# Kernel tuning notes

Measured on AMD Instinct MI355X. Metric: run time of the kernel, lower is better.

Reference implementation:

```python
import jax, jax.numpy as jnp
import numpy as np

B, T, C, H = 4, 2048, 1024, 16
D = C // H


def setup_inputs() -> dict:
    key = jax.random.key(0)
    ks = jax.random.split(key, 6)
    s = 1.0 / np.sqrt(C)
    return {
        "x": jax.random.normal(ks[0], (B, T, C), dtype=jnp.float32),
        "attention_mask": jnp.ones((B, 1, T), dtype=jnp.int32),
        "Wq": jax.random.normal(ks[1], (C, C), dtype=jnp.float32) * s,
        "bq": jnp.zeros((C,), dtype=jnp.float32),
        "Wk": jax.random.normal(ks[2], (C, C), dtype=jnp.float32) * s,
        "bk": jnp.zeros((C,), dtype=jnp.float32),
        "Wv": jax.random.normal(ks[3], (C, C), dtype=jnp.float32) * s,
        "bv": jnp.zeros((C,), dtype=jnp.float32),
        "Wp": jax.random.normal(ks[4], (C, C), dtype=jnp.float32) * s,
        "bp": jnp.zeros((C,), dtype=jnp.float32),
    }


def reference(x, attention_mask, Wq, bq, Wk, bk, Wv, bv, Wp, bp):
    b, t, c = x.shape
    d = c // H
    # projections (torch Linear: x @ W^T + b)
    q = (x @ Wq.T + bq).reshape(b, t, H, d).transpose(0, 2, 1, 3)  # [B,H,T,D]
    k = (x @ Wk.T + bk).reshape(b, t, H, d).transpose(0, 2, 1, 3)
    v = (x @ Wv.T + bv).reshape(b, t, H, d).transpose(0, 2, 1, 3)
    attn = jnp.einsum("bhqd,bhkd->bhqk", q, k) / jnp.sqrt(jnp.asarray(d, x.dtype))
    mask = attention_mask[:, :, :t]  # [B,1,T] -> broadcast over [B,H,T,T] keys
    attn = jnp.where(mask[:, :, None, :] == 0, jnp.asarray(-jnp.inf, x.dtype), attn)
    attn = jax.nn.softmax(attn, axis=-1)  # dropout p=0 (eval)
    y = jnp.einsum("bhqk,bhkd->bhqd", attn, v)
    y = y.transpose(0, 2, 1, 3).reshape(b, t, c)
    return y @ Wp.T + bp
```

## Files before the change

### kernel.cpp

```cpp
#include <hip/hip_runtime.h>


#define TT 2048
#define CC 1024
#define HH 16
#define DD 64
#define BB 4

typedef unsigned short u16;
typedef unsigned int u32;
typedef __attribute__((ext_vector_type(8))) short bf16x8;
typedef __attribute__((ext_vector_type(4))) float f32x4;

#if __has_builtin(__builtin_amdgcn_exp2f)
#define EXP2(x) __builtin_amdgcn_exp2f(x)
#else
#define EXP2(x) __expf((x) * 0.6931471805599453f)
#endif

__device__ __forceinline__ u16 f2bf(float f) {
    u32 u = __builtin_bit_cast(u32, f);
    u += 0x7FFFu + ((u >> 16) & 1u);
    return (u16)(u >> 16);
}
__device__ __forceinline__ u32 pk2(float a, float b) {
    u32 ua = __builtin_bit_cast(u32, a); ua += 0x7FFFu + ((ua >> 16) & 1u);
    u32 ub = __builtin_bit_cast(u32, b); ub += 0x7FFFu + ((ub >> 16) & 1u);
    return __builtin_amdgcn_perm(ub, ua, 0x07060302);
}

#define GLDS(g, l) __builtin_amdgcn_global_load_lds( \
    (const __attribute__((address_space(1))) void*)(g), \
    (__attribute__((address_space(3))) void*)(l), 16, 0, 0)

__global__ __launch_bounds__(256) void wcvt(const float* __restrict__ s,
                                            u16* __restrict__ d, int n8) {
    const int i = blockIdx.x * 256 + threadIdx.x;
    if (i < n8) {
        const float4 f0 = ((const float4*)s)[2 * i];
        const float4 f1 = ((const float4*)s)[2 * i + 1];
        uint4 w;
        w.x = pk2(f0.x, f0.y); w.y = pk2(f0.z, f0.w);
        w.z = pk2(f1.x, f1.y); w.w = pk2(f1.z, f1.w);
        ((uint4*)d)[i] = w;
    }
}

__global__ __launch_bounds__(256) void wcvt3(const float* __restrict__ s0,
                                             const float* __restrict__ s1,
                                             const float* __restrict__ s2,
                                             u16* __restrict__ d0,
                                             u16* __restrict__ d1,
                                             u16* __restrict__ d2, int n8) {
    const int which = blockIdx.y;
    const float* s = (which == 0) ? s0 : (which == 1) ? s1 : s2;
    u16* d = (which == 0) ? d0 : (which == 1) ? d1 : d2;
    const int i = blockIdx.x * 256 + threadIdx.x;
    if (i < n8) {
        const float4 f0 = ((const float4*)s)[2 * i];
        const float4 f1 = ((const float4*)s)[2 * i + 1];
        uint4 w;
        w.x = pk2(f0.x, f0.y); w.y = pk2(f0.z, f0.w);
        w.z = pk2(f1.x, f1.y); w.w = pk2(f1.z, f1.w);
        ((uint4*)d)[i] = w;
    }
}

template <int PROJ>
__global__ __launch_bounds__(256) void gemmX(const u16* __restrict__ A,
                                             const u16* __restrict__ Wb,
                                             const float* __restrict__ b0,
                                             const float* __restrict__ b1,
                                             const float* __restrict__ b2,
                                             void* __restrict__ out0,
                                             void* __restrict__ out1,
                                             void* __restrict__ out2) {
    __shared__ u16 As[128 * 64];
    __shared__ u16 Bs[128 * 64];

    const int tid  = threadIdx.x;
    const int wave = tid >> 6, lane = tid & 63;
    const int quad = lane >> 4, l16 = lane & 15;
    const int bm = blockIdx.y * 128, bn = blockIdx.x * 128;
    const int wm = (wave >> 1) * 64, wn = (wave & 1) * 64;
    const int K = CC;

    f32x4 acc[4][4] = {};

    for (int k0 = 0; k0 < K; k0 += 64) {
#pragma unroll
        for (int rr = 0; rr < 4; rr++) {
            const int c = rr * 256 + tid;
            const int row = c >> 3;
            const int cs = ((c & 7) ^ (row & 7)) * 8;
            GLDS(&Wb[(size_t)(bn + row) * K + k0 + cs], &Bs[c * 8]);
        }
#pragma unroll
        for (int rr = 0; rr < 4; rr++) {
            const int c = rr * 256 + tid;
            const int row = c >> 3;
            const int cs = ((c & 7) ^ (row & 7)) * 8;
            GLDS(&A[(size_t)(bm + row) * K + k0 + cs], &As[c * 8]);
        }
        __syncthreads();

#pragma unroll
        for (int ks = 0; ks < 2; ks++) {
            bf16x8 af[4], bfr[4];
#pragma unroll
            for (int i = 0; i < 4; i++) {
                const int row = wm + i * 16 + l16;
                const int s8 = (ks * 4 + quad) ^ (row & 7);
                af[i] = *(bf16x8*)&As[row * 64 + s8 * 8];
            }
#pragma unroll
            for (int j = 0; j < 4; j++) {
                const int row = wn + j * 16 + l16;
                const int s8 = (ks * 4 + quad) ^ (row & 7);
                bfr[j] = *(bf16x8*)&Bs[row * 64 + s8 * 8];
            }
#pragma unroll
            for (int i = 0; i < 4; i++)
#pragma unroll
                for (int j = 0; j < 4; j++)
                    acc[i][j] = __builtin_amdgcn_mfma_f32_16x16x32_bf16(af[i], bfr[j], acc[i][j], 0, 0, 0);
        }
        __syncthreads();
    }

    if (PROJ) {
        float* out = (float*)out0;
#pragma unroll
        for (int j = 0; j < 4; j++) {
            const int col = bn + wn + j * 16 + l16;
            const float bv = b0[col];
#pragma unroll
            for (int i = 0; i < 4; i++) {
                const int row0 = bm + wm + i * 16 + quad * 4;
#pragma unroll
                for (int r = 0; r < 4; r++)
                    out[(size_t)(row0 + r) * CC + col] = acc[i][j][r] + bv;
            }
        }
    } else {
        const int mid = bn >> 10;
        const float* bias = (mid == 0) ? b0 : (mid == 1) ? b1 : b2;
#pragma unroll
        for (int j = 0; j < 4; j++) {
            const int col  = bn + wn + j * 16 + l16;
            const int colL = col & (CC - 1);
            const float bv = bias[colL];
#pragma unroll
            for (int i = 0; i < 4; i++) {
                const int row0 = bm + wm + i * 16 + quad * 4;
                if (mid < 2) {
                    u16* out = (u16*)(mid ? out1 : out0);
#pragma unroll
                    for (int r = 0; r < 4; r++)
                        out[(size_t)(row0 + r) * CC + colL] = f2bf(acc[i][j][r] + bv);
                } else {
                    const int hh = colL >> 6, dch = colL & 63;
                    const int bb = row0 >> 11, t0 = row0 & (TT - 1);
                    const size_t idx = (((size_t)bb * HH + hh) * DD + dch) * TT + t0;
                    uint2 w;
                    w.x = pk2(acc[i][j][0] + bv, acc[i][j][1] + bv);
                    w.y = pk2(acc[i][j][2] + bv, acc[i][j][3] + bv);
                    *(uint2*)&((u16*)out2)[idx] = w;
                }
            }
        }
    }
}

__global__ __launch_bounds__(256) void attn(const u16* __restrict__ Q,
                                            const u16* __restrict__ Kb,
                                            const u16* __restrict__ Vt,
                                            const int* __restrict__ mask,
                                            u16* __restrict__ Y) {
    const int b = blockIdx.z, h = blockIdx.y, qt = blockIdx.x;
    const int tid  = threadIdx.x;
    const int wave = tid >> 6, lane = tid & 63;
    const int quad = lane >> 4, l16 = lane & 15;
    const int qrow0 = qt * 128 + wave * 32;

    __shared__ u16 Ks[64 * 64];
    __shared__ u16 Vs[64 * 64];
    __shared__ u16 Plds[4][32][72];

    const size_t qb = ((size_t)b * TT + qrow0) * CC + h * DD;

    bf16x8 qf[2][2];
#pragma unroll
    for (int m = 0; m < 2; m++)
#pragma unroll
        for (int ks = 0; ks < 2; ks++)
            qf[m][ks] = *(const bf16x8*)&Q[qb + (size_t)(m * 16 + l16) * CC + ks * 32 + quad * 8];

    const int c0 = tid, c1 = tid + 256;
    const int r0 = c0 >> 3, r1 = c1 >> 3;
    const int kp0 = (c0 & 7) ^ ((r0 >> 2) & 7), kp1 = (c1 & 7) ^ ((r1 >> 2) & 7);
    const int vp0 = (c0 & 7) ^ (r0 & 7),        vp1 = (c1 & 7) ^ (r1 & 7);
    const u16* kgp = Kb + ((size_t)b * TT) * CC + h * DD;
    const u16* vgp = Vt + ((size_t)(b * HH + h) * DD) * TT;
    const int* mp = mask + b * TT + 4 * l16;

    f32x4 o[2][4] = {};
    float lsum[2][4] = {};
    const float SC = 0.18033688011112042f;

#pragma unroll 1
    for (int kt = 0; kt < TT; kt += 64) {
        GLDS(&kgp[(size_t)(kt + r0) * CC + kp0 * 8], &Ks[c0 * 8]);
        GLDS(&kgp[(size_t)(kt + r1) * CC + kp1 * 8], &Ks[c1 * 8]);
        GLDS(&vgp[(size_t)r0 * TT + kt + vp0 * 8], &Vs[c0 * 8]);
        GLDS(&vgp[(size_t)r1 * TT + kt + vp1 * 8], &Vs[c1 * 8]);
        __syncthreads();

        f32x4 s[2][4] = {};
#pragma unroll
        for (int n = 0; n < 4; n++) {
#pragma unroll
            for (int ks = 0; ks < 2; ks++) {
                const int krow = 4 * l16 + n;
                const int pos = (ks * 4 + quad) ^ ((krow >> 2) & 7);
                const bf16x8 kf = *(bf16x8*)&Ks[krow * 64 + pos * 8];
#pragma unroll
                for (int m = 0; m < 2; m++)
                    s[m][n] = __builtin_amdgcn_mfma_f32_16x16x32_bf16(qf[m][ks], kf, s[m][n], 0, 0, 0);
            }
        }

        const int4 mv = *(const int4*)&mp[kt];
        float bb[4];
        bb[0] = mv.x ? 0.f : -1e38f;
        bb[1] = mv.y ? 0.f : -1e38f;
        bb[2] = mv.z ? 0.f : -1e38f;
        bb[3] = mv.w ? 0.f : -1e38f;

#pragma unroll
        for (int m = 0; m < 2; m++)
#pragma unroll
            for (int r = 0; r < 4; r++) {
                const float p0 = EXP2(fmaf(s[m][0][r], SC, bb[0]));
                const float p1 = EXP2(fmaf(s[m][1][r], SC, bb[1]));
                const float p2 = EXP2(fmaf(s[m][2][r], SC, bb[2]));
                const float p3 = EXP2(fmaf(s[m][3][r], SC, bb[3]));
                lsum[m][r] += (p0 + p1) + (p2 + p3);
                uint2 w; w.x = pk2(p0, p1); w.y = pk2(p2, p3);
                *(uint2*)&Plds[wave][m * 16 + quad * 4 + r][4 * l16] = w;
            }

#pragma unroll
        for (int ks = 0; ks < 2; ks++) {
            bf16x8 pf[2];
#pragma unroll
            for (int m = 0; m < 2; m++)
                pf[m] = *(bf16x8*)&Plds[wave][m * 16 + l16][ks * 32 + quad * 8];
#pragma unroll
            for (int dt = 0; dt < 4; dt++) {
                const int vrow = dt * 16 + l16;
                const int pos = (ks * 4 + quad) ^ (vrow & 7);
                const bf16x8 vf = *(bf16x8*)&Vs[vrow * 64 + pos * 8];
#pragma unroll
                for (int m = 0; m < 2; m++)
                    o[m][dt] = __builtin_amdgcn_mfma_f32_16x16x32_bf16(pf[m], vf, o[m][dt], 0, 0, 0);
            }
        }
        __syncthreads();
    }

#pragma unroll
    for (int off = 1; off < 16; off <<= 1)
#pragma unroll
        for (int m = 0; m < 2; m++)
#pragma unroll
            for (int r = 0; r < 4; r++) lsum[m][r] += __shfl_xor(lsum[m][r], off, 64);

#pragma unroll
    for (int m = 0; m < 2; m++) {
        float inv[4];
#pragma unroll
        for (int r = 0; r < 4; r++) inv[r] = 1.0f / lsum[m][r];
#pragma unroll
        for (int dt = 0; dt < 4; dt++)
#pragma unroll
            for (int r = 0; r < 4; r++)
                Y[qb + (size_t)(m * 16 + quad * 4 + r) * CC + dt * 16 + l16] = f2bf(o[m][dt][r] * inv[r]);
    }
}

extern "C" void kernel_launch(void* const* d_in, const int* in_sizes, int n_in,
                              void* d_out, int out_size, void* d_ws, size_t ws_size,
                              hipStream_t stream) {
    const float* x    = (const float*)d_in[0];
    const int*   mask = (const int*)d_in[1];
    const float* Wq   = (const float*)d_in[2];
    const float* bq   = (const float*)d_in[3];
    const float* Wk   = (const float*)d_in[4];
    const float* bk   = (const float*)d_in[5];
    const float* Wv   = (const float*)d_in[6];
    const float* bv   = (const float*)d_in[7];
    const float* Wp   = (const float*)d_in[8];
    const float* bp   = (const float*)d_in[9];

    u16* ws = (u16*)d_ws;
    const size_t sz = (size_t)BB * TT * CC;
    u16* Qb   = ws;
    u16* Kbuf = ws + sz;
    u16* Vtb  = ws + 2 * sz;

    u16* xb   = (u16*)d_out;
    u16* Wq16 = xb + sz;
    u16* Wk16 = Wq16 + (size_t)CC * CC;
    u16* Wv16 = Wk16 + (size_t)CC * CC;

    const int W8 = CC * CC / 8;
    wcvt<<<4096, 256, 0, stream>>>(x, xb, (int)(sz / 8));
    wcvt3<<<dim3(512, 3), 256, 0, stream>>>(Wq, Wk, Wv, Wq16, Wk16, Wv16, W8);

    gemmX<0><<<dim3(24, 64), 256, 0, stream>>>(xb, Wq16, bq, bk, bv, Qb, Kbuf, Vtb);

    attn<<<dim3(TT / 128, HH, BB), 256, 0, stream>>>(Qb, Kbuf, Vtb, mask, Qb);

    wcvt<<<512, 256, 0, stream>>>(Wp, Kbuf, W8);
    gemmX<1><<<dim3(8, 64), 256, 0, stream>>>(Qb, Kbuf, bp, nullptr, nullptr, d_out, nullptr, nullptr);
}
```

Measured before the change: 331.6 us.

## Double-buffer K/V tiles in attention loop and raise MFMA wave priority

The attention kernel now uses two LDS buffers for K and V. The next tile is prefetched with global-to-LDS loads while the current tile is consumed, so there is one barrier per iteration and the load latency overlaps with compute. The MFMA sections are also wrapped in s_setprio to favour matrix issue. LDS use grows, which may lower occupancy. The explicit vmcnt waits and barriers must keep the buffer hazards correct.

```diff
diff --git a/kernel.cpp b/kernel.cpp
--- a/kernel.cpp
+++ b/kernel.cpp
@@ -183,8 +183,8 @@
     const int quad = lane >> 4, l16 = lane & 15;
     const int qrow0 = qt * 128 + wave * 32;
 
-    __shared__ u16 Ks[64 * 64];
-    __shared__ u16 Vs[64 * 64];
+    __shared__ u16 Ks[2][64 * 64];
+    __shared__ u16 Vs[2][64 * 64];
     __shared__ u16 Plds[4][32][72];
 
     const size_t qb = ((size_t)b * TT + qrow0) * CC + h * DD;
@@ -208,29 +208,46 @@
     float lsum[2][4] = {};
     const float SC = 0.18033688011112042f;
 
+    GLDS(&kgp[(size_t)r0 * CC + kp0 * 8], &Ks[0][c0 * 8]);
+    GLDS(&kgp[(size_t)r1 * CC + kp1 * 8], &Ks[0][c1 * 8]);
+    GLDS(&vgp[(size_t)r0 * TT + vp0 * 8], &Vs[0][c0 * 8]);
+    GLDS(&vgp[(size_t)r1 * TT + vp1 * 8], &Vs[0][c1 * 8]);
+    asm volatile("s_waitcnt vmcnt(0)" ::: "memory");
+    __builtin_amdgcn_s_barrier();
+    __builtin_amdgcn_sched_barrier(0);
+
 #pragma unroll 1
     for (int kt = 0; kt < TT; kt += 64) {
-        GLDS(&kgp[(size_t)(kt + r0) * CC + kp0 * 8], &Ks[c0 * 8]);
-        GLDS(&kgp[(size_t)(kt + r1) * CC + kp1 * 8], &Ks[c1 * 8]);
-        GLDS(&vgp[(size_t)r0 * TT + kt + vp0 * 8], &Vs[c0 * 8]);
-        GLDS(&vgp[(size_t)r1 * TT + kt + vp1 * 8], &Vs[c1 * 8]);
-        __syncthreads();
+        const int cur = (kt >> 6) & 1;
+        const u16* Kc = &Ks[cur][0];
+        const u16* Vc = &Vs[cur][0];
+
+        const int4 mv = *(const int4*)&mp[kt];
+
+        if (kt + 64 < TT) {
+            const int nxt = cur ^ 1;
+            GLDS(&kgp[(size_t)(kt + 64 + r0) * CC + kp0 * 8], &Ks[nxt][c0 * 8]);
+            GLDS(&kgp[(size_t)(kt + 64 + r1) * CC + kp1 * 8], &Ks[nxt][c1 * 8]);
+            GLDS(&vgp[(size_t)r0 * TT + kt + 64 + vp0 * 8], &Vs[nxt][c0 * 8]);
+            GLDS(&vgp[(size_t)r1 * TT + kt + 64 + vp1 * 8], &Vs[nxt][c1 * 8]);
+        }
 
         f32x4 s[2][4] = {};
+        __builtin_amdgcn_s_setprio(1);
 #pragma unroll
         for (int n = 0; n < 4; n++) {
 #pragma unroll
             for (int ks = 0; ks < 2; ks++) {
                 const int krow = 4 * l16 + n;
                 const int pos = (ks * 4 + quad) ^ ((krow >> 2) & 7);
-                const bf16x8 kf = *(bf16x8*)&Ks[krow * 64 + pos * 8];
+                const bf16x8 kf = *(bf16x8*)&Kc[krow * 64 + pos * 8];
 #pragma unroll
                 for (int m = 0; m < 2; m++)
                     s[m][n] = __builtin_amdgcn_mfma_f32_16x16x32_bf16(qf[m][ks], kf, s[m][n], 0, 0, 0);
             }
         }
-
-        const int4 mv = *(const int4*)&mp[kt];
+        __builtin_amdgcn_s_setprio(0);
+
         float bb[4];
         bb[0] = mv.x ? 0.f : -1e38f;
         bb[1] = mv.y ? 0.f : -1e38f;
@@ -250,6 +267,7 @@
                 *(uint2*)&Plds[wave][m * 16 + quad * 4 + r][4 * l16] = w;
             }
 
+        __builtin_amdgcn_s_setprio(1);
 #pragma unroll
         for (int ks = 0; ks < 2; ks++) {
             bf16x8 pf[2];
@@ -260,13 +278,17 @@
             for (int dt = 0; dt < 4; dt++) {
                 const int vrow = dt * 16 + l16;
                 const int pos = (ks * 4 + quad) ^ (vrow & 7);
-                const bf16x8 vf = *(bf16x8*)&Vs[vrow * 64 + pos * 8];
+                const bf16x8 vf = *(bf16x8*)&Vc[vrow * 64 + pos * 8];
 #pragma unroll
                 for (int m = 0; m < 2; m++)
                     o[m][dt] = __builtin_amdgcn_mfma_f32_16x16x32_bf16(pf[m], vf, o[m][dt], 0, 0, 0);
             }
         }
-        __syncthreads();
+        __builtin_amdgcn_s_setprio(0);
+
+        asm volatile("s_waitcnt vmcnt(0)" ::: "memory");
+        __builtin_amdgcn_sched_barrier(0);
+        __builtin_amdgcn_s_barrier();
     }
 
 #pragma unroll
```

After: 310.3 us. 6.4% less time.
